# Performance work log

Measured on AMD Instinct MI355X. Metric: run time of the kernel, lower is better.

## Reference

```python
import jax, jax.numpy as jnp
import numpy as np

N, E, D, R = 50000, 600000, 128, 500


def setup_inputs() -> dict:
    key = jax.random.key(0)
    ks = jax.random.split(key, 9)
    h = jax.random.normal(ks[0], (N, D), dtype=jnp.float32)
    norm = jax.random.uniform(ks[1], (N, 1), dtype=jnp.float32)
    emb_rel = jax.random.normal(ks[2], (R, D), dtype=jnp.float32)
    scale = 1.0 / np.sqrt(D)  # xavier-ish scale for DxD weights
    weight_neighbor = jax.random.normal(ks[3], (D, D), dtype=jnp.float32) * scale
    loop_weight = jax.random.normal(ks[4], (D, D), dtype=jnp.float32) * scale
    evolve_loop_weight = jax.random.normal(ks[5], (D, D), dtype=jnp.float32) * scale
    src = jax.random.randint(ks[6], (E,), 0, N, dtype=jnp.int32)
    dst = jax.random.randint(ks[7], (E,), 0, N, dtype=jnp.int32)
    etype = jax.random.randint(ks[8], (E,), 0, R, dtype=jnp.int32)
    return {
        "h": h, "norm": norm, "emb_rel": emb_rel,
        "weight_neighbor": weight_neighbor, "loop_weight": loop_weight,
        "evolve_loop_weight": evolve_loop_weight,
        "src": src, "dst": dst, "etype": etype,
    }


def reference(h, norm, emb_rel, weight_neighbor, loop_weight,
              evolve_loop_weight, src, dst, etype):
    # msg_func: gather src node features + relation embeddings, add, dense matmul
    msg = (h[src] + emb_rel[etype]) @ weight_neighbor        # [E, D]
    # update_all(fn.sum): scatter-sum messages into destination nodes
    agg = jax.ops.segment_sum(msg, dst, num_segments=N)       # [N, D]
    # apply_func: scale by per-node norm
    h_agg = agg * norm                                        # [N, D]
    # self-loop: nodes with in-degree > 0 use loop_weight, others evolve_loop_weight
    in_deg = jax.ops.segment_sum(jnp.ones((E,), dtype=jnp.float32), dst,
                                 num_segments=N)              # [N]
    loop_msg = jnp.where((in_deg > 0)[:, None],
                         h @ loop_weight,
                         h @ evolve_loop_weight)              # [N, D]
    node_repr = h_agg + loop_msg
    return jax.nn.relu(node_repr)
```

## Files before the change

kernel.cpp:

```cpp
#include <hip/hip_runtime.h>
#include <hip/hip_bf16.h>


#define DIM 128
#define MAXD 64

typedef __attribute__((ext_vector_type(8))) short bf16x8_t;
typedef __attribute__((ext_vector_type(4))) float f32x4_t;

__device__ inline ushort f2bf(float f) {
    __hip_bfloat16 b = __float2bfloat16(f);
    return *reinterpret_cast<ushort*>(&b);
}
__device__ inline float blo(unsigned u) { return __uint_as_float(u << 16); }
__device__ inline float bhi(unsigned u) { return __uint_as_float(u & 0xffff0000u); }
__device__ inline uint4 cvt8(const float4& a, const float4& b) {
    uint4 o;
    o.x = f2bf(a.x) | ((unsigned)f2bf(a.y) << 16);
    o.y = f2bf(a.z) | ((unsigned)f2bf(a.w) << 16);
    o.z = f2bf(b.x) | ((unsigned)f2bf(b.y) << 16);
    o.w = f2bf(b.z) | ((unsigned)f2bf(b.w) << 16);
    return o;
}

__global__ __launch_bounds__(256) void init_kernel(
    const float4* __restrict__ h4, const float4* __restrict__ emb4,
    const float* __restrict__ Wn, const float* __restrict__ Wl,
    uint4* __restrict__ h8, uint4* __restrict__ emb8,
    ushort* __restrict__ Bpack, int* __restrict__ cursor,
    int* __restrict__ zcount, int nH8, int nE8, int N)
{
    int i = blockIdx.x * 256 + threadIdx.x;
    if (i < nH8) {
        h8[i] = cvt8(h4[2 * i], h4[2 * i + 1]);
        return;
    }
    int j = i - nH8;
    if (j < 16) { h8[nH8 + j] = make_uint4(0, 0, 0, 0); return; }
    j -= 16;
    if (j < nE8) {
        emb8[j] = cvt8(emb4[2 * j], emb4[2 * j + 1]);
        return;
    }
    j -= nE8;
    if (j < 16) { emb8[nE8 + j] = make_uint4(0, 0, 0, 0); return; }
    j -= 16;
    if (j < 32768) {
        int jj   = j & 7;
        int lane = (j >> 3) & 63;
        int ks   = (j >> 9) & 7;
        int nt   = j >> 12;
        int k = ks * 32 + (lane >> 4) * 8 + jj;
        int n = nt * 16 + (lane & 15);
        float v = (k < DIM) ? Wn[k * DIM + n] : Wl[(k - DIM) * DIM + n];
        Bpack[j] = f2bf(v);
        return;
    }
    j -= 32768;
    if (j < N) { cursor[j] = 0; return; }
    if (j == N) *zcount = 0;
}

__global__ __launch_bounds__(256) void fill_kernel(
    const int4* __restrict__ src4, const int4* __restrict__ dst4,
    const int4* __restrict__ et4, int* __restrict__ cursor,
    unsigned* __restrict__ region, int E4,
    const int* __restrict__ src, const int* __restrict__ dst,
    const int* __restrict__ etype, int E)
{
    int i = blockIdx.x * 256 + threadIdx.x;
    if (i < E4) {
        int4 s = src4[i], d = dst4[i], t = et4[i];
        int p;
        p = atomicAdd(cursor + d.x, 1);
        region[d.x * MAXD + p] = (unsigned)s.x | ((unsigned)t.x << 17);
        p = atomicAdd(cursor + d.y, 1);
        region[d.y * MAXD + p] = (unsigned)s.y | ((unsigned)t.y << 17);
        p = atomicAdd(cursor + d.z, 1);
        region[d.z * MAXD + p] = (unsigned)s.z | ((unsigned)t.z << 17);
        p = atomicAdd(cursor + d.w, 1);
        region[d.w * MAXD + p] = (unsigned)s.w | ((unsigned)t.w << 17);
    }
    if (i == 0)
        for (int e = E4 * 4; e < E; ++e) {
            int p = atomicAdd(cursor + dst[e], 1);
            region[dst[e] * MAXD + p] = (unsigned)src[e] | ((unsigned)etype[e] << 17);
        }
}

__device__ inline void addbf8(float2* a, uint4 hv, uint4 rv) {
    a[0].x += blo(hv.x) + blo(rv.x); a[0].y += bhi(hv.x) + bhi(rv.x);
    a[1].x += blo(hv.y) + blo(rv.y); a[1].y += bhi(hv.y) + bhi(rv.y);
    a[2].x += blo(hv.z) + blo(rv.z); a[2].y += bhi(hv.z) + bhi(rv.z);
    a[3].x += blo(hv.w) + blo(rv.w); a[3].y += bhi(hv.w) + bhi(rv.w);
}

__global__ __launch_bounds__(256) void gather_kernel(
    const uint4* __restrict__ h8,
    const uint4* __restrict__ emb8,
    const float* __restrict__ norm,
    const int* __restrict__ cursor,
    const unsigned* __restrict__ region,
    uint4* __restrict__ aggn8,
    int* __restrict__ zcount, int* __restrict__ zlist,
    int N, unsigned SENT)
{
    int n = blockIdx.x * 16 + (threadIdx.x >> 4);
    if (n >= N) return;
    int lane = threadIdx.x & 15;
    int cnt = cursor[n];

    if (cnt == 0) {
        if (lane == 0) {
            int p = atomicAdd(zcount, 1);
            zlist[p] = n;
        }
        aggn8[(size_t)n * 16 + lane] = make_uint4(0, 0, 0, 0);
        return;
    }

    float nm = norm[n];
    const unsigned* reg = region + (size_t)n * MAXD;
    float2 a[4];
    a[0] = a[1] = a[2] = a[3] = make_float2(0.f, 0.f);

    for (int k = 0; k < cnt; k += 4) {
        uint4 r = *(const uint4*)(reg + k);
        unsigned w0 = r.x;
        unsigned w1 = (k + 1 < cnt) ? r.y : SENT;
        unsigned w2 = (k + 2 < cnt) ? r.z : SENT;
        unsigned w3 = (k + 3 < cnt) ? r.w : SENT;
        uint4 h0 = h8[(size_t)(w0 & 0x1FFFF) * 16 + lane];
        uint4 e0 = emb8[(size_t)(w0 >> 17) * 16 + lane];
        uint4 h1 = h8[(size_t)(w1 & 0x1FFFF) * 16 + lane];
        uint4 e1 = emb8[(size_t)(w1 >> 17) * 16 + lane];
        uint4 h2 = h8[(size_t)(w2 & 0x1FFFF) * 16 + lane];
        uint4 e2 = emb8[(size_t)(w2 >> 17) * 16 + lane];
        uint4 h3 = h8[(size_t)(w3 & 0x1FFFF) * 16 + lane];
        uint4 e3 = emb8[(size_t)(w3 >> 17) * 16 + lane];
        addbf8(a, h0, e0);
        addbf8(a, h1, e1);
        addbf8(a, h2, e2);
        addbf8(a, h3, e3);
    }

    uint4 o;
    o.x = f2bf(a[0].x * nm) | ((unsigned)f2bf(a[0].y * nm) << 16);
    o.y = f2bf(a[1].x * nm) | ((unsigned)f2bf(a[1].y * nm) << 16);
    o.z = f2bf(a[2].x * nm) | ((unsigned)f2bf(a[2].y * nm) << 16);
    o.w = f2bf(a[3].x * nm) | ((unsigned)f2bf(a[3].y * nm) << 16);
    aggn8[(size_t)n * 16 + lane] = o;
}

__global__ __launch_bounds__(256) void mfma_gemm_kernel(
    const ushort* __restrict__ aggn_bf,
    const ushort* __restrict__ h_bf,
    const ushort* __restrict__ Bpack,
    float* __restrict__ out,
    int nRowTiles, int halfWaves)
{
    int wave = threadIdx.x >> 6;
    int lane = threadIdx.x & 63;
    int wid  = blockIdx.x * 4 + wave;
    int ch   = wid & 1;
    int w    = wid >> 1;
    int m    = lane & 15;
    int quad = lane >> 4;

    bf16x8_t b[4][8];
    #pragma unroll
    for (int nt = 0; nt < 4; ++nt)
        #pragma unroll
        for (int ks = 0; ks < 8; ++ks)
            b[nt][ks] = *(const bf16x8_t*)(Bpack +
                (((size_t)(ch * 4 + nt) * 8 + ks) * 64 + lane) * 8);

    for (int rt = w; rt < nRowTiles; rt += halfWaves) {
        size_t rowOff = (size_t)(rt * 16 + m) * DIM + quad * 8;
        bf16x8_t a[8];
        #pragma unroll
        for (int ks = 0; ks < 4; ++ks) {
            a[ks]     = *(const bf16x8_t*)(aggn_bf + rowOff + ks * 32);
            a[ks + 4] = *(const bf16x8_t*)(h_bf   + rowOff + ks * 32);
        }
        f32x4_t acc[4];
        #pragma unroll
        for (int nt = 0; nt < 4; ++nt)
            #pragma unroll
            for (int r = 0; r < 4; ++r) acc[nt][r] = 0.f;

        #pragma unroll
        for (int ks = 0; ks < 8; ++ks)
            #pragma unroll
            for (int nt = 0; nt < 4; ++nt)
                acc[nt] = __builtin_amdgcn_mfma_f32_16x16x32_bf16(
                    a[ks], b[nt][ks], acc[nt], 0, 0, 0);

        int colBase = ch * 64 + m;
        int rowBase = rt * 16 + quad * 4;
        #pragma unroll
        for (int nt = 0; nt < 4; ++nt)
            #pragma unroll
            for (int r = 0; r < 4; ++r)
                out[(size_t)(rowBase + r) * DIM + colBase + nt * 16] =
                    fmaxf(acc[nt][r], 0.f);
    }
}

__global__ __launch_bounds__(128) void fixup_kernel(
    const float* __restrict__ h, const float* __restrict__ We,
    const int* __restrict__ zlist, const int* __restrict__ zcount,
    float* __restrict__ out)
{
    int cnt = *zcount;
    int c = threadIdx.x;
    for (int i = blockIdx.x; i < cnt; i += gridDim.x) {
        int n = zlist[i];
        float s = 0.f;
        for (int k = 0; k < DIM; ++k)
            s = fmaf(h[(size_t)n * DIM + k], We[(size_t)k * DIM + c], s);
        out[(size_t)n * DIM + c] = fmaxf(s, 0.f);
    }
}

extern "C" void kernel_launch(void* const* d_in, const int* in_sizes, int n_in,
                              void* d_out, int out_size, void* d_ws, size_t ws_size,
                              hipStream_t stream)
{
    const float* h    = (const float*)d_in[0];
    const float* norm = (const float*)d_in[1];
    const float* emb  = (const float*)d_in[2];
    const float* Wn   = (const float*)d_in[3];
    const float* Wl   = (const float*)d_in[4];
    const float* We   = (const float*)d_in[5];
    const int* src    = (const int*)d_in[6];
    const int* dst    = (const int*)d_in[7];
    const int* etype  = (const int*)d_in[8];

    const int N = in_sizes[1];
    const int E = in_sizes[6];
    const int R = in_sizes[2] / DIM;

    char* p = (char*)d_ws;
    ushort*   h_bf    = (ushort*)p;    p += (size_t)(N + 1) * DIM * 2;
    ushort*   emb_bf  = (ushort*)p;    p += (size_t)(R + 1) * DIM * 2;
    ushort*   Bpack   = (ushort*)p;    p += 2 * DIM * DIM * 2;
    ushort*   aggn_bf = (ushort*)p;    p += (size_t)N * DIM * 2;
    unsigned* region  = (unsigned*)p;  p += (size_t)N * MAXD * 4;
    int*      cursor  = (int*)p;       p += ((size_t)N * 4 + 15) & ~(size_t)15;
    int*      zcount  = (int*)p;       p += 16;
    int*      zlist   = (int*)p;

    const int nH8 = N * DIM / 8;
    const int nE8 = R * DIM / 8;
    const int initTotal = nH8 + 16 + nE8 + 16 + 32768 + N + 1;
    const unsigned SENT = (unsigned)N | ((unsigned)R << 17);

    init_kernel<<<dim3((initTotal + 255) / 256), dim3(256), 0, stream>>>(
        (const float4*)h, (const float4*)emb, Wn, Wl,
        (uint4*)h_bf, (uint4*)emb_bf, Bpack, cursor, zcount, nH8, nE8, N);

    fill_kernel<<<dim3((E / 4 + 255) / 256), dim3(256), 0, stream>>>(
        (const int4*)src, (const int4*)dst, (const int4*)etype,
        cursor, region, E / 4, src, dst, etype, E);

    gather_kernel<<<dim3((N + 15) / 16), dim3(256), 0, stream>>>(
        (const uint4*)h_bf, (const uint4*)emb_bf, norm, cursor, region,
        (uint4*)aggn_bf, zcount, zlist, N, SENT);

    const int nRowTiles = (N + 15) / 16;
    mfma_gemm_kernel<<<dim3(512), dim3(256), 0, stream>>>(
        aggn_bf, h_bf, Bpack, (float*)d_out, nRowTiles, 1024);

    fixup_kernel<<<dim3(2), dim3(128), 0, stream>>>(
        h, We, zlist, zcount, (float*)d_out);
}
```

Before: 168.4 us.

## Slice bf16 feature tables into 8 column slabs for cache-local gathers

Stores the bf16 node and relation tables, and the aggregated output, as 8 column slices of 16 features each. The gather kernel now runs one slice per block, so each slice's table (about 1.6 MB) has a better chance of staying resident in L2 across random src lookups. The MFMA GEMM reads its A operands through the new sliced layout. The cost is 8x more reads of the region index list, 8-byte per-lane loads in place of 16-byte ones, and more blocks launched.

```diff
diff --git a/kernel.cpp b/kernel.cpp
--- a/kernel.cpp
+++ b/kernel.cpp
@@ -28,22 +28,32 @@
     const float* __restrict__ Wn, const float* __restrict__ Wl,
     uint4* __restrict__ h8, uint4* __restrict__ emb8,
     ushort* __restrict__ Bpack, int* __restrict__ cursor,
-    int* __restrict__ zcount, int nH8, int nE8, int N)
+    int* __restrict__ zcount, int nH8, int nE8, int N, int R)
 {
     int i = blockIdx.x * 256 + threadIdx.x;
     if (i < nH8) {
-        h8[i] = cvt8(h4[2 * i], h4[2 * i + 1]);
+        int n = i >> 4, s = (i & 15) >> 1, hh = i & 1;
+        h8[((size_t)s * (N + 1) + n) * 2 + hh] = cvt8(h4[2 * i], h4[2 * i + 1]);
         return;
     }
     int j = i - nH8;
-    if (j < 16) { h8[nH8 + j] = make_uint4(0, 0, 0, 0); return; }
+    if (j < 16) {
+        int s = j >> 1, hh = j & 1;
+        h8[((size_t)s * (N + 1) + N) * 2 + hh] = make_uint4(0, 0, 0, 0);
+        return;
+    }
     j -= 16;
     if (j < nE8) {
-        emb8[j] = cvt8(emb4[2 * j], emb4[2 * j + 1]);
+        int n = j >> 4, s = (j & 15) >> 1, hh = j & 1;
+        emb8[((size_t)s * (R + 1) + n) * 2 + hh] = cvt8(emb4[2 * j], emb4[2 * j + 1]);
         return;
     }
     j -= nE8;
-    if (j < 16) { emb8[nE8 + j] = make_uint4(0, 0, 0, 0); return; }
+    if (j < 16) {
+        int s = j >> 1, hh = j & 1;
+        emb8[((size_t)s * (R + 1) + R) * 2 + hh] = make_uint4(0, 0, 0, 0);
+        return;
+    }
     j -= 16;
     if (j < 32768) {
         int jj   = j & 7;
@@ -88,41 +98,35 @@
         }
 }
 
-__device__ inline void addbf8(float2* a, uint4 hv, uint4 rv) {
-    a[0].x += blo(hv.x) + blo(rv.x); a[0].y += bhi(hv.x) + bhi(rv.x);
-    a[1].x += blo(hv.y) + blo(rv.y); a[1].y += bhi(hv.y) + bhi(rv.y);
-    a[2].x += blo(hv.z) + blo(rv.z); a[2].y += bhi(hv.z) + bhi(rv.z);
-    a[3].x += blo(hv.w) + blo(rv.w); a[3].y += bhi(hv.w) + bhi(rv.w);
-}
-
 __global__ __launch_bounds__(256) void gather_kernel(
-    const uint4* __restrict__ h8,
-    const uint4* __restrict__ emb8,
+    const uint2* __restrict__ h2,
+    const uint2* __restrict__ e2,
     const float* __restrict__ norm,
     const int* __restrict__ cursor,
     const unsigned* __restrict__ region,
-    uint4* __restrict__ aggn8,
+    uint2* __restrict__ aggn2,
     int* __restrict__ zcount, int* __restrict__ zlist,
-    int N, unsigned SENT)
-{
-    int n = blockIdx.x * 16 + (threadIdx.x >> 4);
+    int N, int R, unsigned SENT)
+{
+    int s  = blockIdx.x & 7;
+    int nb = blockIdx.x >> 3;
+    int n  = nb * 64 + (threadIdx.x >> 2);
     if (n >= N) return;
-    int lane = threadIdx.x & 15;
+    int l  = threadIdx.x & 3;
     int cnt = cursor[n];
+    uint2* aout = aggn2 + ((size_t)s * N + n) * 4 + l;
 
     if (cnt == 0) {
-        if (lane == 0) {
-            int p = atomicAdd(zcount, 1);
-            zlist[p] = n;
-        }
-        aggn8[(size_t)n * 16 + lane] = make_uint4(0, 0, 0, 0);
-        return;
-    }
-
+        if (s == 0 && l == 0) { int p = atomicAdd(zcount, 1); zlist[p] = n; }
+        *aout = make_uint2(0, 0);
+        return;
+    }
+
+    const uint2* hsl = h2 + (size_t)s * (N + 1) * 4 + l;
+    const uint2* esl = e2 + (size_t)s * (R + 1) * 4 + l;
+    const unsigned* reg = region + (size_t)n * MAXD;
     float nm = norm[n];
-    const unsigned* reg = region + (size_t)n * MAXD;
-    float2 a[4];
-    a[0] = a[1] = a[2] = a[3] = make_float2(0.f, 0.f);
+    float a0 = 0.f, a1 = 0.f, a2 = 0.f, a3 = 0.f;
 
     for (int k = 0; k < cnt; k += 4) {
         uint4 r = *(const uint4*)(reg + k);
@@ -130,26 +134,28 @@
         unsigned w1 = (k + 1 < cnt) ? r.y : SENT;
         unsigned w2 = (k + 2 < cnt) ? r.z : SENT;
         unsigned w3 = (k + 3 < cnt) ? r.w : SENT;
-        uint4 h0 = h8[(size_t)(w0 & 0x1FFFF) * 16 + lane];
-        uint4 e0 = emb8[(size_t)(w0 >> 17) * 16 + lane];
-        uint4 h1 = h8[(size_t)(w1 & 0x1FFFF) * 16 + lane];
-        uint4 e1 = emb8[(size_t)(w1 >> 17) * 16 + lane];
-        uint4 h2 = h8[(size_t)(w2 & 0x1FFFF) * 16 + lane];
-        uint4 e2 = emb8[(size_t)(w2 >> 17) * 16 + lane];
-        uint4 h3 = h8[(size_t)(w3 & 0x1FFFF) * 16 + lane];
-        uint4 e3 = emb8[(size_t)(w3 >> 17) * 16 + lane];
-        addbf8(a, h0, e0);
-        addbf8(a, h1, e1);
-        addbf8(a, h2, e2);
-        addbf8(a, h3, e3);
-    }
-
-    uint4 o;
-    o.x = f2bf(a[0].x * nm) | ((unsigned)f2bf(a[0].y * nm) << 16);
-    o.y = f2bf(a[1].x * nm) | ((unsigned)f2bf(a[1].y * nm) << 16);
-    o.z = f2bf(a[2].x * nm) | ((unsigned)f2bf(a[2].y * nm) << 16);
-    o.w = f2bf(a[3].x * nm) | ((unsigned)f2bf(a[3].y * nm) << 16);
-    aggn8[(size_t)n * 16 + lane] = o;
+        uint2 hv0 = hsl[(size_t)(w0 & 0x1FFFF) * 4];
+        uint2 ev0 = esl[(size_t)(w0 >> 17) * 4];
+        uint2 hv1 = hsl[(size_t)(w1 & 0x1FFFF) * 4];
+        uint2 ev1 = esl[(size_t)(w1 >> 17) * 4];
+        uint2 hv2 = hsl[(size_t)(w2 & 0x1FFFF) * 4];
+        uint2 ev2 = esl[(size_t)(w2 >> 17) * 4];
+        uint2 hv3 = hsl[(size_t)(w3 & 0x1FFFF) * 4];
+        uint2 ev3 = esl[(size_t)(w3 >> 17) * 4];
+        a0 += blo(hv0.x) + blo(ev0.x); a1 += bhi(hv0.x) + bhi(ev0.x);
+        a2 += blo(hv0.y) + blo(ev0.y); a3 += bhi(hv0.y) + bhi(ev0.y);
+        a0 += blo(hv1.x) + blo(ev1.x); a1 += bhi(hv1.x) + bhi(ev1.x);
+        a2 += blo(hv1.y) + blo(ev1.y); a3 += bhi(hv1.y) + bhi(ev1.y);
+        a0 += blo(hv2.x) + blo(ev2.x); a1 += bhi(hv2.x) + bhi(ev2.x);
+        a2 += blo(hv2.y) + blo(ev2.y); a3 += bhi(hv2.y) + bhi(ev2.y);
+        a0 += blo(hv3.x) + blo(ev3.x); a1 += bhi(hv3.x) + bhi(ev3.x);
+        a2 += blo(hv3.y) + blo(ev3.y); a3 += bhi(hv3.y) + bhi(ev3.y);
+    }
+
+    uint2 o;
+    o.x = f2bf(a0 * nm) | ((unsigned)f2bf(a1 * nm) << 16);
+    o.y = f2bf(a2 * nm) | ((unsigned)f2bf(a3 * nm) << 16);
+    *aout = o;
 }
 
 __global__ __launch_bounds__(256) void mfma_gemm_kernel(
@@ -157,7 +163,7 @@
     const ushort* __restrict__ h_bf,
     const ushort* __restrict__ Bpack,
     float* __restrict__ out,
-    int nRowTiles, int halfWaves)
+    int nRowTiles, int halfWaves, int N)
 {
     int wave = threadIdx.x >> 6;
     int lane = threadIdx.x & 63;
@@ -166,6 +172,8 @@
     int w    = wid >> 1;
     int m    = lane & 15;
     int quad = lane >> 4;
+    int sq   = quad >> 1;
+    int off8 = (quad & 1) * 8;
 
     bf16x8_t b[4][8];
     #pragma unroll
@@ -176,12 +184,15 @@
                 (((size_t)(ch * 4 + nt) * 8 + ks) * 64 + lane) * 8);
 
     for (int rt = w; rt < nRowTiles; rt += halfWaves) {
-        size_t rowOff = (size_t)(rt * 16 + m) * DIM + quad * 8;
+        int row = rt * 16 + m;
         bf16x8_t a[8];
         #pragma unroll
         for (int ks = 0; ks < 4; ++ks) {
-            a[ks]     = *(const bf16x8_t*)(aggn_bf + rowOff + ks * 32);
-            a[ks + 4] = *(const bf16x8_t*)(h_bf   + rowOff + ks * 32);
+            int s = 2 * ks + sq;
+            a[ks]     = *(const bf16x8_t*)(aggn_bf +
+                            ((size_t)s * N + row) * 16 + off8);
+            a[ks + 4] = *(const bf16x8_t*)(h_bf +
+                            ((size_t)s * (N + 1) + row) * 16 + off8);
         }
         f32x4_t acc[4];
         #pragma unroll
@@ -258,19 +269,20 @@
 
     init_kernel<<<dim3((initTotal + 255) / 256), dim3(256), 0, stream>>>(
         (const float4*)h, (const float4*)emb, Wn, Wl,
-        (uint4*)h_bf, (uint4*)emb_bf, Bpack, cursor, zcount, nH8, nE8, N);
+        (uint4*)h_bf, (uint4*)emb_bf, Bpack, cursor, zcount, nH8, nE8, N, R);
 
     fill_kernel<<<dim3((E / 4 + 255) / 256), dim3(256), 0, stream>>>(
         (const int4*)src, (const int4*)dst, (const int4*)etype,
         cursor, region, E / 4, src, dst, etype, E);
 
-    gather_kernel<<<dim3((N + 15) / 16), dim3(256), 0, stream>>>(
-        (const uint4*)h_bf, (const uint4*)emb_bf, norm, cursor, region,
-        (uint4*)aggn_bf, zcount, zlist, N, SENT);
+    const int nodeBlocks = (N + 63) / 64;
+    gather_kernel<<<dim3(nodeBlocks * 8), dim3(256), 0, stream>>>(
+        (const uint2*)h_bf, (const uint2*)emb_bf, norm, cursor, region,
+        (uint2*)aggn_bf, zcount, zlist, N, R, SENT);
 
     const int nRowTiles = (N + 15) / 16;
     mfma_gemm_kernel<<<dim3(512), dim3(256), 0, stream>>>(
-        aggn_bf, h_bf, Bpack, (float*)d_out, nRowTiles, 1024);
+        aggn_bf, h_bf, Bpack, (float*)d_out, nRowTiles, 1024, N);
 
     fixup_kernel<<<dim3(2), dim3(128), 0, stream>>>(
         h, We, zlist, zcount, (float*)d_out);
```

Result: slower. 191.8 us (+13.9%).
